# Performance work log

Hardware: AMD Instinct MI355X
Metric: run time of the kernel (lower is better)

The kernel has to match this reference:

```python
import math
import jax, jax.numpy as jnp
import numpy as np

B, N, CS, CZ, C, H, PQ, PV = 1, 768, 384, 128, 16, 12, 4, 8
INF, EPS = 100000.0, 1e-8
CONCAT = H * (CZ + C + PV * 4)  # 2112


def setup_inputs() -> dict:
    key = jax.random.key(0)
    ks = jax.random.split(key, 16)
    # random proper rotations via QR (numpy, deterministic)
    rng = np.random.default_rng(0)
    m = rng.standard_normal((B * N, 3, 3)).astype(np.float32)
    q, r = np.linalg.qr(m)
    q = q * np.sign(np.diagonal(r, axis1=-2, axis2=-1))[:, None, :]
    rot = jnp.asarray(q.reshape(B, N, 3, 3), dtype=jnp.float32)

    def lin(k, fin, fout):
        return jax.random.normal(k, (fin, fout), jnp.float32) / math.sqrt(fin)

    return {
        "s": jax.random.normal(ks[0], (B, N, CS), jnp.float32),
        "z": jax.random.normal(ks[1], (B, N, N, CZ), jnp.float32),
        "rot": rot,
        "trans": jax.random.normal(ks[2], (B, N, 3), jnp.float32),
        "mask": jnp.ones((B, N), jnp.float32),
        "Wq": lin(ks[3], CS, H * C), "bq": jnp.zeros((H * C,), jnp.float32),
        "Wkv": lin(ks[4], CS, 2 * H * C), "bkv": jnp.zeros((2 * H * C,), jnp.float32),
        "Wqp": lin(ks[5], CS, H * PQ * 3), "bqp": jnp.zeros((H * PQ * 3,), jnp.float32),
        "Wkvp": lin(ks[6], CS, H * (PQ + PV) * 3), "bkvp": jnp.zeros((H * (PQ + PV) * 3,), jnp.float32),
        "Wb": lin(ks[7], CZ, H), "bb": jnp.zeros((H,), jnp.float32),
        "head_w": jnp.full((H,), 0.541324854612918, jnp.float32),  # softplus^-1(1)
        "Wout": lin(ks[8], CONCAT, CS), "bout": jnp.zeros((CS,), jnp.float32),
    }


def reference(s, z, rot, trans, mask, Wq, bq, Wkv, bkv, Wqp, bqp, Wkvp, bkvp, Wb, bb, head_w, Wout, bout):
    q = (s @ Wq + bq).reshape(B, N, H, C)
    kv = (s @ Wkv + bkv).reshape(B, N, H, 2 * C)
    k, v = kv[..., :C], kv[..., C:]

    def to_points(lin_out, P):
        # torch split-into-3 + stack(dim=-1) layout: [.., 3, H*P] -> [.., H*P, 3]
        pts = lin_out.reshape(B, N, 3, H * P).swapaxes(-1, -2)
        pts = jnp.einsum('bnxy,bnpy->bnpx', rot, pts) + trans[:, :, None, :]
        return pts.reshape(B, N, H, P, 3)

    q_pts = to_points(s @ Wqp + bqp, PQ)
    kv_pts = to_points(s @ Wkvp + bkvp, PQ + PV)
    k_pts, v_pts = kv_pts[..., :PQ, :], kv_pts[..., PQ:, :]

    b = z @ Wb + bb  # [B,N,N,H]
    a = jnp.einsum('bihc,bjhc->bhij', q, k) * math.sqrt(1.0 / (3 * C))
    a = a + math.sqrt(1.0 / 3) * jnp.transpose(b, (0, 3, 1, 2))

    # point-distance attention: [B,N,N,H,PQ]
    d2 = jnp.sum((q_pts[:, :, None] - k_pts[:, None]) ** 2, axis=-1)
    hw = jax.nn.softplus(head_w) * math.sqrt(1.0 / (3 * (PQ * 9.0 / 2)))
    pt_att = -0.5 * jnp.sum(d2 * hw[:, None], axis=-1)  # [B,N,N,H]
    sq_mask = INF * (mask[:, :, None] * mask[:, None, :] - 1.0)
    a = a + jnp.transpose(pt_att, (0, 3, 1, 2)) + sq_mask[:, None]
    a = jax.nn.softmax(a, axis=-1)  # [B,H,N,N]

    o = jnp.einsum('bhij,bjhc->bihc', a, v).reshape(B, N, H * C)
    o_pt = jnp.einsum('bhij,bjhpx->bihpx', a, v_pts)  # [B,N,H,PV,3]
    # invert_apply: R^T (x - t)
    o_pt = jnp.einsum('bnyx,bnhpy->bnhpx', rot, o_pt - trans[:, :, None, None, :])
    o_pt_norm = jnp.sqrt(jnp.sum(o_pt ** 2, axis=-1) + EPS).reshape(B, N, H * PV)
    o_pt_flat = o_pt.reshape(B, N, H * PV, 3)
    o_pair = jnp.einsum('bhij,bijc->bihc', a, z).reshape(B, N, H * CZ)

    cat = jnp.concatenate(
        [o, o_pt_flat[..., 0], o_pt_flat[..., 1], o_pt_flat[..., 2], o_pt_norm, o_pair], axis=-1)
    return cat @ Wout + bout
```

## Files before the change

kernel.cpp:

```cpp
#include <hip/hip_runtime.h>
#include <math.h>

#define NN 768
#define CSn 384
#define CZn 128
#define Hn 12
#define CONCATn 2112
#define LGS 772

__global__ __launch_bounds__(256, 4) void projbias_kernel(
    const float* __restrict__ s,
    const float* __restrict__ Wq, const float* __restrict__ bq,
    const float* __restrict__ Wkv, const float* __restrict__ bkv,
    const float* __restrict__ Wqp, const float* __restrict__ bqp,
    const float* __restrict__ Wkvp, const float* __restrict__ bkvp,
    float* __restrict__ linG,
    const float* __restrict__ z, const float* __restrict__ Wb,
    const float* __restrict__ bb, float* __restrict__ bG)
{
    __shared__ float sl[16 * 388];
    __shared__ float wbs[1536];
    const int bid = blockIdx.x;
    const int t = threadIdx.x;

    if (bid < 864) {
        const int rt = bid % 48, ct = bid / 48;
        const int r0 = rt * 16;
        for (int x4 = t; x4 < 1536; x4 += 256) {
            const int r = x4 / 96, c4 = x4 % 96;
            *(float4*)&sl[r * 388 + c4 * 4] = *(const float4*)(s + (size_t)(r0 + r) * CSn + c4 * 4);
        }
        __syncthreads();
        const int c = t & 63, rq = t >> 6;
        const int col = ct * 64 + c;
        const float* Wp; int fout; float bias;
        if (col < 192)      { Wp = Wq + col;         fout = 192; bias = bq[col]; }
        else if (col < 576) { Wp = Wkv + (col-192);  fout = 384; bias = bkv[col-192]; }
        else if (col < 720) { Wp = Wqp + (col-576);  fout = 144; bias = bqp[col-576]; }
        else                { Wp = Wkvp + (col-720); fout = 432; bias = bkvp[col-720]; }
        float a0=bias, a1=bias, a2=bias, a3=bias;
        const float* s0 = sl + (rq*4+0)*388;
        const float* s1 = sl + (rq*4+1)*388;
        const float* s2 = sl + (rq*4+2)*388;
        const float* s3 = sl + (rq*4+3)*388;
        float wA[8], wB[8];
        #pragma unroll
        for (int u = 0; u < 8; ++u) wA[u] = Wp[(size_t)u * fout];
        #pragma unroll 1
        for (int kk = 0; kk < 384; kk += 16) {
            #pragma unroll
            for (int u = 0; u < 8; ++u) wB[u] = Wp[(size_t)(kk + 8 + u) * fout];
            #pragma unroll
            for (int u = 0; u < 8; ++u) {
                const float wv = wA[u];
                a0 += s0[kk+u]*wv; a1 += s1[kk+u]*wv;
                a2 += s2[kk+u]*wv; a3 += s3[kk+u]*wv;
            }
            if (kk + 16 < 384) {
                #pragma unroll
                for (int u = 0; u < 8; ++u) wA[u] = Wp[(size_t)(kk + 16 + u) * fout];
            }
            #pragma unroll
            for (int u = 0; u < 8; ++u) {
                const float wv = wB[u];
                a0 += s0[kk+8+u]*wv; a1 += s1[kk+8+u]*wv;
                a2 += s2[kk+8+u]*wv; a3 += s3[kk+8+u]*wv;
            }
        }
        float* lr = linG + (size_t)(r0 + rq*4) * 1152 + col;
        lr[0] = a0; lr[1152] = a1; lr[2*1152] = a2; lr[3*1152] = a3;
    } else {
        const int bb2 = bid - 864;
        const int jt = bb2 % 12, i = bb2 / 12;
        for (int x = t; x < 1536; x += 256) wbs[x] = Wb[(x & 127)*12 + (x >> 7)];
        __syncthreads();

        const int jl = t >> 2, g = t & 3;
        const int j = jt * 64 + jl;
        const float* zr = z + ((size_t)i * NN + j) * CZn + g * 4;
        float4 zv[8];
        #pragma unroll
        for (int u = 0; u < 8; ++u) zv[u] = *(const float4*)(zr + u * 16);

        float bh[12];
        #pragma unroll
        for (int h = 0; h < 12; ++h) bh[h] = 0.f;
        #pragma unroll
        for (int u = 0; u < 8; ++u) {
            const float* wb = wbs + u*16 + g*4;
            #pragma unroll
            for (int h = 0; h < 12; ++h) {
                const float4 wv = *(const float4*)(wb + h * 128);
                bh[h] += zv[u].x*wv.x + zv[u].y*wv.y + zv[u].z*wv.z + zv[u].w*wv.w;
            }
        }
        #pragma unroll
        for (int h = 0; h < 12; ++h) {
            bh[h] += __shfl_xor(bh[h], 1);
            bh[h] += __shfl_xor(bh[h], 2);
        }
        float bsel[3];
        #pragma unroll
        for (int hh = 0; hh < 3; ++hh) {
            const float v01 = (g & 1) ? bh[3+hh] : bh[0+hh];
            const float v23 = (g & 1) ? bh[9+hh] : bh[6+hh];
            bsel[hh] = (g & 2) ? v23 : v01;
        }
        float* bgr = bG + (size_t)i * (Hn*NN) + j;
        #pragma unroll
        for (int hh = 0; hh < 3; ++hh) {
            const int h = 3*g + hh;
            bgr[(size_t)h * NN] = 0.5773502691896258f * (bsel[hh] + bb[h]);
        }
    }
}

__global__ __launch_bounds__(256) void scatter_kernel(
    const float* __restrict__ linG, const float* __restrict__ rot, const float* __restrict__ trans,
    float* __restrict__ q, float* __restrict__ kT, float* __restrict__ v,
    float* __restrict__ qp, float* __restrict__ kpT, float* __restrict__ vp)
{
    const int i = blockIdx.x, t = threadIdx.x;
    const float* lr = linG + (size_t)i * 1152;
    if (t < 192) q[(size_t)i*192 + t] = lr[t];
    for (int tt = t; tt < 384; tt += 256) {
        const int h = tt >> 5, cc = tt & 31;
        const float val = lr[192 + tt];
        if (cc < 16) kT[(size_t)(h*16 + cc)*NN + i] = val;
        else         v[(size_t)i*192 + h*16 + (cc-16)] = val;
    }
    const float R0 = rot[i*9+0], R1 = rot[i*9+1], R2 = rot[i*9+2];
    const float R3 = rot[i*9+3], R4 = rot[i*9+4], R5 = rot[i*9+5];
    const float R6 = rot[i*9+6], R7 = rot[i*9+7], R8 = rot[i*9+8];
    const float T0 = trans[i*3+0], T1 = trans[i*3+1], T2 = trans[i*3+2];
    if (t < 48) {
        const float px = lr[576 + t], py = lr[576 + 48 + t], pz = lr[576 + 96 + t];
        float* d = qp + (size_t)i*144 + t*3;
        d[0] = R0*px + R1*py + R2*pz + T0;
        d[1] = R3*px + R4*py + R5*pz + T1;
        d[2] = R6*px + R7*py + R8*pz + T2;
    }
    if (t < 144) {
        const float px = lr[720 + t], py = lr[720 + 144 + t], pz = lr[720 + 288 + t];
        const float gx = R0*px + R1*py + R2*pz + T0;
        const float gy = R3*px + R4*py + R5*pz + T1;
        const float gz = R6*px + R7*py + R8*pz + T2;
        const int h = t / 12, pp = t % 12;
        if (pp < 4) {
            float* d = kpT + (size_t)(h*12 + pp*3)*NN + i;
            d[0] = gx; d[NN] = gy; d[2*NN] = gz;
        } else {
            float* d = vp + (size_t)i*288 + ((h*8) + (pp-4))*3;
            d[0] = gx; d[1] = gy; d[2] = gz;
        }
    }
}

#define LOADG(KV, KPV, BGv, MJv, uu) {                                        \
    const int jo_ = (uu) * 64;                                                \
    _Pragma("unroll") for (int c_ = 0; c_ < 16; ++c_)                         \
        KV[c_] = kb[(size_t)c_*NN + jo_];                                     \
    _Pragma("unroll") for (int e_ = 0; e_ < 12; ++e_)                         \
        KPV[e_] = kpb[(size_t)e_*NN + jo_];                                   \
    BGv = bgb[jo_]; MJv = mask[l + jo_]; }

#define COMPG(KV, KPV, BGv, MJv, uu) {                                        \
    float qk_ = 0.f;                                                          \
    _Pragma("unroll") for (int c_ = 0; c_ < 16; ++c_) qk_ += qreg[c_]*KV[c_]; \
    float d2_ = 0.f;                                                          \
    _Pragma("unroll") for (int e_ = 0; e_ < 12; ++e_) {                       \
        const float d_ = qpreg[e_] - KPV[e_]; d2_ += d_*d_; }                 \
    e[uu] = 0.14433756729740643f*qk_ + BGv + coef*d2_                         \
          + 100000.0f*(mi*MJv - 1.0f); }

__global__ __launch_bounds__(256, 3) void mega_kernel(
    const float* __restrict__ mask,
    const float* __restrict__ q, const float* __restrict__ qp,
    const float* __restrict__ kT, const float* __restrict__ kpT,
    const float* __restrict__ bG, const float* __restrict__ head_w,
    const float* __restrict__ z,
    const float* __restrict__ v, const float* __restrict__ vp,
    const float* __restrict__ rot, const float* __restrict__ trans,
    float* __restrict__ cat)
{
    const int i = blockIdx.x, t = threadIdx.x;
    const int w = t >> 6, l = t & 63;
    __shared__ float lg[Hn * LGS];
    __shared__ float qs[192], qps[144], coefS[12];
    __shared__ float pts[288];
    if (t < 192) qs[t] = q[(size_t)i*192 + t];
    if (t < 144) qps[t] = qp[(size_t)i*144 + t];
    if (t < 12) coefS[t] = -0.5f * 0.1360827634879543f * log1pf(expf(head_w[t]));
    __syncthreads();
    const float mi = mask[i];

    #pragma unroll 1
    for (int hh = 0; hh < 3; ++hh) {
        const int h = w*3 + hh;
        float qreg[16], qpreg[12];
        #pragma unroll
        for (int c = 0; c < 16; ++c) qreg[c] = qs[h*16 + c];
        #pragma unroll
        for (int ee = 0; ee < 12; ++ee) qpreg[ee] = qps[h*12 + ee];
        const float coef = coefS[h];
        const float* kb  = kT  + (size_t)(h*16)*NN + l;
        const float* kpb = kpT + (size_t)(h*12)*NN + l;
        const float* bgb = bG + (size_t)i*(Hn*NN) + (size_t)h*NN + l;
        float e[12];
        float kvA[16], kpvA[12], bgA, mjA;
        float kvB[16], kpvB[12], bgB, mjB;
        LOADG(kvA, kpvA, bgA, mjA, 0);
        #pragma unroll
        for (int u = 0; u < 12; u += 2) {
            LOADG(kvB, kpvB, bgB, mjB, u + 1);
            COMPG(kvA, kpvA, bgA, mjA, u);
            if (u + 2 < 12) LOADG(kvA, kpvA, bgA, mjA, u + 2);
            COMPG(kvB, kpvB, bgB, mjB, u + 1);
        }
        float m = -1e30f;
        #pragma unroll
        for (int u = 0; u < 12; ++u) m = fmaxf(m, e[u]);
        #pragma unroll
        for (int off = 32; off > 0; off >>= 1) m = fmaxf(m, __shfl_xor(m, off));
        float ssum = 0.f;
        #pragma unroll
        for (int u = 0; u < 12; ++u) { e[u] = expf(e[u] - m); ssum += e[u]; }
        #pragma unroll
        for (int off = 32; off > 0; off >>= 1) ssum += __shfl_xor(ssum, off);
        const float inv = 1.0f / ssum;
        #pragma unroll
        for (int u = 0; u < 12; ++u) lg[h*LGS + l + u*64] = e[u] * inv;
    }
    __syncthreads();

    {
        float accA = 0.f;
        const float* srcA; int strA; int hA;
        if (t < 192) { srcA = v + t;          strA = 192; hA = t >> 4; }
        else         { srcA = vp + (t - 192); strA = 288; hA = (t - 192) / 24; }
        const float* arA = lg + hA * LGS;
        {
            float vA[8], vB[8];
            #pragma unroll
            for (int u = 0; u < 8; ++u) vA[u] = srcA[(size_t)u * strA];
            #pragma unroll 1
            for (int jb = 0; jb < NN; jb += 16) {
                #pragma unroll
                for (int u = 0; u < 8; ++u) vB[u] = srcA[(size_t)(jb + 8 + u) * strA];
                #pragma unroll
                for (int u = 0; u < 8; ++u) accA += arA[jb + u] * vA[u];
                if (jb + 16 < NN) {
                    #pragma unroll
                    for (int u = 0; u < 8; ++u) vA[u] = srcA[(size_t)(jb + 16 + u) * strA];
                }
                #pragma unroll
                for (int u = 0; u < 8; ++u) accA += arA[jb + 8 + u] * vB[u];
            }
        }
        float accB = 0.f;
        if (t < 224) {
            const int cB = 64 + t;
            const float* srcB = vp + cB;
            const float* arB = lg + (cB / 24) * LGS;
            float vA[8], vB[8];
            #pragma unroll
            for (int u = 0; u < 8; ++u) vA[u] = srcB[(size_t)u * 288];
            #pragma unroll 1
            for (int jb = 0; jb < NN; jb += 16) {
                #pragma unroll
                for (int u = 0; u < 8; ++u) vB[u] = srcB[(size_t)(jb + 8 + u) * 288];
                #pragma unroll
                for (int u = 0; u < 8; ++u) accB += arB[jb + u] * vA[u];
                if (jb + 16 < NN) {
                    #pragma unroll
                    for (int u = 0; u < 8; ++u) vA[u] = srcB[(size_t)(jb + 16 + u) * 288];
                }
                #pragma unroll
                for (int u = 0; u < 8; ++u) accB += arB[jb + 8 + u] * vB[u];
            }
        }
        float* catr = cat + (size_t)i*CONCATn;
        if (t < 192) catr[t] = accA;
        else         pts[t - 192] = accA;
        if (t < 224) pts[64 + t] = accB;
    }
    __syncthreads();

    if (t < 96) {
        const float gx = pts[t*3+0] - trans[i*3+0];
        const float gy = pts[t*3+1] - trans[i*3+1];
        const float gz = pts[t*3+2] - trans[i*3+2];
        const float lx = rot[i*9+0]*gx + rot[i*9+3]*gy + rot[i*9+6]*gz;
        const float ly = rot[i*9+1]*gx + rot[i*9+4]*gy + rot[i*9+7]*gz;
        const float lz = rot[i*9+2]*gx + rot[i*9+5]*gy + rot[i*9+8]*gz;
        float* catr = cat + (size_t)i*CONCATn;
        catr[192 + t] = lx;
        catr[288 + t] = ly;
        catr[384 + t] = lz;
        catr[480 + t] = sqrtf(lx*lx + ly*ly + lz*lz + 1e-8f);
    }

    {
        const int c4 = l & 31, jp = l >> 5;
        const float* zb = z + (size_t)i*NN*CZn + c4*4;
        const float* a0 = lg + (size_t)(3*w + 0)*LGS;
        const float* a1 = lg + (size_t)(3*w + 1)*LGS;
        const float* a2 = lg + (size_t)(3*w + 2)*LGS;
        float x00=0.f,x01=0.f,x02=0.f,x03=0.f;
        float x10=0.f,x11=0.f,x12=0.f,x13=0.f;
        float x20=0.f,x21=0.f,x22=0.f,x23=0.f;
        float4 zA[8], zB[8];
        #pragma unroll
        for (int u = 0; u < 8; ++u)
            zA[u] = *(const float4*)(zb + (size_t)(2*u + jp)*CZn);
        #pragma unroll 1
        for (int jb = 0; jb < 384; jb += 16) {
            #pragma unroll
            for (int u = 0; u < 8; ++u)
                zB[u] = *(const float4*)(zb + (size_t)(2*(jb + 8 + u) + jp)*CZn);
            #pragma unroll
            for (int u = 0; u < 8; ++u) {
                const int j = 2*(jb + u) + jp;
                const float4 zv = zA[u];
                const float A0 = a0[j], A1 = a1[j], A2 = a2[j];
                x00 += A0*zv.x; x01 += A0*zv.y; x02 += A0*zv.z; x03 += A0*zv.w;
                x10 += A1*zv.x; x11 += A1*zv.y; x12 += A1*zv.z; x13 += A1*zv.w;
                x20 += A2*zv.x; x21 += A2*zv.y; x22 += A2*zv.z; x23 += A2*zv.w;
            }
            if (jb + 16 < 384) {
                #pragma unroll
                for (int u = 0; u < 8; ++u)
                    zA[u] = *(const float4*)(zb + (size_t)(2*(jb + 16 + u) + jp)*CZn);
            }
            #pragma unroll
            for (int u = 0; u < 8; ++u) {
                const int j = 2*(jb + 8 + u) + jp;
                const float4 zv = zB[u];
                const float A0 = a0[j], A1 = a1[j], A2 = a2[j];
                x00 += A0*zv.x; x01 += A0*zv.y; x02 += A0*zv.z; x03 += A0*zv.w;
                x10 += A1*zv.x; x11 += A1*zv.y; x12 += A1*zv.z; x13 += A1*zv.w;
                x20 += A2*zv.x; x21 += A2*zv.y; x22 += A2*zv.z; x23 += A2*zv.w;
            }
        }
        x00 += __shfl_xor(x00, 32); x01 += __shfl_xor(x01, 32);
        x02 += __shfl_xor(x02, 32); x03 += __shfl_xor(x03, 32);
        x10 += __shfl_xor(x10, 32); x11 += __shfl_xor(x11, 32);
        x12 += __shfl_xor(x12, 32); x13 += __shfl_xor(x13, 32);
        x20 += __shfl_xor(x20, 32); x21 += __shfl_xor(x21, 32);
        x22 += __shfl_xor(x22, 32); x23 += __shfl_xor(x23, 32);
        if (jp == 0) {
            float* cr = cat + (size_t)i*CONCATn + 576 + c4*4;
            float4 r0; r0.x=x00; r0.y=x01; r0.z=x02; r0.w=x03;
            float4 r1; r1.x=x10; r1.y=x11; r1.z=x12; r1.w=x13;
            float4 r2; r2.x=x20; r2.y=x21; r2.z=x22; r2.w=x23;
            *(float4*)(cr + (size_t)(3*w+0)*CZn) = r0;
            *(float4*)(cr + (size_t)(3*w+1)*CZn) = r1;
            *(float4*)(cr + (size_t)(3*w+2)*CZn) = r2;
        }
    }
}

__global__ __launch_bounds__(128) void outpart_kernel(
    const float* __restrict__ cat, const float* __restrict__ Wout,
    float* __restrict__ pbuf)
{
    const int rt = blockIdx.x;
    const int ot = blockIdx.y;
    const int qt = blockIdx.z;
    __shared__ float cl[4 * 528];
    const int r0 = rt * 4;
    const int kb = qt * 528;
    for (int idx = threadIdx.x; idx < 528; idx += 128) {
        const int r = idx / 132, c4 = idx % 132;
        *(float4*)&cl[r*528 + c4*4] =
            *(const float4*)(cat + (size_t)(r0 + r)*CONCATn + kb + c4*4);
    }
    __syncthreads();
    const int t = threadIdx.x;
    const int r  = t >> 5;
    const int o4 = t & 31;
    const int col = ot * 128 + o4 * 4;
    float4 acc; acc.x = 0.f; acc.y = 0.f; acc.z = 0.f; acc.w = 0.f;
    const float* wp = Wout + (size_t)kb * 384 + col;
    const float* cr = cl + r * 528;
    float4 wA[8], wB[8];
    #pragma unroll
    for (int u = 0; u < 8; ++u) wA[u] = *(const float4*)(wp + (size_t)u * 384);
    #pragma unroll 1
    for (int kk = 0; kk < 528; kk += 16) {
        #pragma unroll
        for (int u = 0; u < 8; ++u)
            wB[u] = *(const float4*)(wp + (size_t)(kk + 8 + u) * 384);
        #pragma unroll
        for (int u = 0; u < 8; ++u) {
            const float cv = cr[kk + u];
            acc.x += cv * wA[u].x; acc.y += cv * wA[u].y;
            acc.z += cv * wA[u].z; acc.w += cv * wA[u].w;
        }
        if (kk + 16 < 528) {
            #pragma unroll
            for (int u = 0; u < 8; ++u)
                wA[u] = *(const float4*)(wp + (size_t)(kk + 16 + u) * 384);
        }
        #pragma unroll
        for (int u = 0; u < 8; ++u) {
            const float cv = cr[kk + 8 + u];
            acc.x += cv * wB[u].x; acc.y += cv * wB[u].y;
            acc.z += cv * wB[u].z; acc.w += cv * wB[u].w;
        }
    }
    *(float4*)(pbuf + ((size_t)qt*NN + r0 + r)*384 + col) = acc;
}

__global__ __launch_bounds__(256) void outfin_kernel(
    const float* __restrict__ pbuf, const float* __restrict__ bout,
    float* __restrict__ out)
{
    const int idx4 = blockIdx.x * 256 + threadIdx.x;
    const int Q = NN * 384 / 4;
    const float4 p0 = ((const float4*)pbuf)[idx4];
    const float4 p1 = ((const float4*)pbuf)[idx4 + Q];
    const float4 p2 = ((const float4*)pbuf)[idx4 + 2*Q];
    const float4 p3 = ((const float4*)pbuf)[idx4 + 3*Q];
    const float4 bo = *(const float4*)(bout + (idx4 % 96) * 4);
    float4 r;
    r.x = p0.x + p1.x + p2.x + p3.x + bo.x;
    r.y = p0.y + p1.y + p2.y + p3.y + bo.y;
    r.z = p0.z + p1.z + p2.z + p3.z + bo.z;
    r.w = p0.w + p1.w + p2.w + p3.w + bo.w;
    ((float4*)out)[idx4] = r;
}

extern "C" void kernel_launch(void* const* d_in, const int* in_sizes, int n_in,
                              void* d_out, int out_size, void* d_ws, size_t ws_size,
                              hipStream_t stream)
{
    const float* s     = (const float*)d_in[0];
    const float* z     = (const float*)d_in[1];
    const float* rot   = (const float*)d_in[2];
    const float* trans = (const float*)d_in[3];
    const float* mask  = (const float*)d_in[4];
    const float* Wq    = (const float*)d_in[5];
    const float* bq    = (const float*)d_in[6];
    const float* Wkv   = (const float*)d_in[7];
    const float* bkv   = (const float*)d_in[8];
    const float* Wqp   = (const float*)d_in[9];
    const float* bqp   = (const float*)d_in[10];
    const float* Wkvp  = (const float*)d_in[11];
    const float* bkvp  = (const float*)d_in[12];
    const float* Wb    = (const float*)d_in[13];
    const float* bb    = (const float*)d_in[14];
    const float* head_w= (const float*)d_in[15];
    const float* Wout  = (const float*)d_in[16];
    const float* bout  = (const float*)d_in[17];
    float* out = (float*)d_out;

    float* ws    = (float*)d_ws;
    float* q     = ws;
    float* kT    = q     + 147456;
    float* qp    = kT    + 147456;
    float* kpT   = qp    + 110592;
    float* v     = kpT   + 110592;
    float* vp    = v     + 147456;
    float* cat   = vp    + 221184;
    float* linG  = cat   + 1622016;
    float* bG    = linG  + 884736;
    float* pbuf  = bG    + 7077888;

    hipLaunchKernelGGL(projbias_kernel, dim3(864 + 12*768), dim3(256), 0, stream,
        s, Wq, bq, Wkv, bkv, Wqp, bqp, Wkvp, bkvp, linG, z, Wb, bb, bG);
    hipLaunchKernelGGL(scatter_kernel, dim3(768), dim3(256), 0, stream,
        linG, rot, trans, q, kT, v, qp, kpT, vp);
    hipLaunchKernelGGL(mega_kernel, dim3(768), dim3(256), 0, stream,
        mask, q, qp, kT, kpT, bG, head_w, z, v, vp, rot, trans, cat);
    hipLaunchKernelGGL(outpart_kernel, dim3(192, 3, 4), dim3(128), 0, stream,
        cat, Wout, pbuf);
    hipLaunchKernelGGL(outfin_kernel, dim3(288), dim3(256), 0, stream,
        pbuf, bout, out);
}
```

Measured before the change: 352.4 us.

## Write q/k/v directly from projection kernel and simplify z-pair loop

The projection GEMM epilogue now writes q, transposed k, and v straight to their final layouts, so the scatter kernel handles only the point projections and linG shrinks to the point columns. This removes one global round trip for the scalar q/k/v data. Separately, the manual double-buffered z prefetch in the pair-output loop is replaced with a plain loop unrolled by 8, leaving load scheduling to the compiler. That lowers register pressure but may expose more memory latency. The kT writes from the epilogue are 4-wide contiguous per thread but strided across threads.

```diff
diff --git a/kernel.cpp b/kernel.cpp
--- a/kernel.cpp
+++ b/kernel.cpp
@@ -14,6 +14,7 @@
     const float* __restrict__ Wkv, const float* __restrict__ bkv,
     const float* __restrict__ Wqp, const float* __restrict__ bqp,
     const float* __restrict__ Wkvp, const float* __restrict__ bkvp,
+    float* __restrict__ q, float* __restrict__ kT, float* __restrict__ v,
     float* __restrict__ linG,
     const float* __restrict__ z, const float* __restrict__ Wb,
     const float* __restrict__ bb, float* __restrict__ bG)
@@ -67,8 +68,28 @@
                 a2 += s2[kk+8+u]*wv; a3 += s3[kk+8+u]*wv;
             }
         }
-        float* lr = linG + (size_t)(r0 + rq*4) * 1152 + col;
-        lr[0] = a0; lr[1152] = a1; lr[2*1152] = a2; lr[3*1152] = a3;
+        const int rb = r0 + rq*4;
+        if (col < 192) {
+            q[(size_t)(rb+0)*192 + col] = a0;
+            q[(size_t)(rb+1)*192 + col] = a1;
+            q[(size_t)(rb+2)*192 + col] = a2;
+            q[(size_t)(rb+3)*192 + col] = a3;
+        } else if (col < 576) {
+            const int tt = col - 192, h = tt >> 5, cc = tt & 31;
+            if (cc < 16) {
+                float* d = kT + (size_t)(h*16 + cc)*NN + rb;
+                d[0] = a0; d[1] = a1; d[2] = a2; d[3] = a3;
+            } else {
+                const int vc = h*16 + (cc - 16);
+                v[(size_t)(rb+0)*192 + vc] = a0;
+                v[(size_t)(rb+1)*192 + vc] = a1;
+                v[(size_t)(rb+2)*192 + vc] = a2;
+                v[(size_t)(rb+3)*192 + vc] = a3;
+            }
+        } else {
+            float* lr = linG + (size_t)rb * 576 + (col - 576);
+            lr[0] = a0; lr[576] = a1; lr[2*576] = a2; lr[3*576] = a3;
+        }
     } else {
         const int bb2 = bid - 864;
         const int jt = bb2 % 12, i = bb2 / 12;
@@ -115,33 +136,25 @@
     }
 }
 
-__global__ __launch_bounds__(256) void scatter_kernel(
+__global__ __launch_bounds__(256) void pts_scatter_kernel(
     const float* __restrict__ linG, const float* __restrict__ rot, const float* __restrict__ trans,
-    float* __restrict__ q, float* __restrict__ kT, float* __restrict__ v,
     float* __restrict__ qp, float* __restrict__ kpT, float* __restrict__ vp)
 {
     const int i = blockIdx.x, t = threadIdx.x;
-    const float* lr = linG + (size_t)i * 1152;
-    if (t < 192) q[(size_t)i*192 + t] = lr[t];
-    for (int tt = t; tt < 384; tt += 256) {
-        const int h = tt >> 5, cc = tt & 31;
-        const float val = lr[192 + tt];
-        if (cc < 16) kT[(size_t)(h*16 + cc)*NN + i] = val;
-        else         v[(size_t)i*192 + h*16 + (cc-16)] = val;
-    }
+    const float* lr = linG + (size_t)i * 576;
     const float R0 = rot[i*9+0], R1 = rot[i*9+1], R2 = rot[i*9+2];
     const float R3 = rot[i*9+3], R4 = rot[i*9+4], R5 = rot[i*9+5];
     const float R6 = rot[i*9+6], R7 = rot[i*9+7], R8 = rot[i*9+8];
     const float T0 = trans[i*3+0], T1 = trans[i*3+1], T2 = trans[i*3+2];
     if (t < 48) {
-        const float px = lr[576 + t], py = lr[576 + 48 + t], pz = lr[576 + 96 + t];
+        const float px = lr[t], py = lr[48 + t], pz = lr[96 + t];
         float* d = qp + (size_t)i*144 + t*3;
         d[0] = R0*px + R1*py + R2*pz + T0;
         d[1] = R3*px + R4*py + R5*pz + T1;
         d[2] = R6*px + R7*py + R8*pz + T2;
     }
     if (t < 144) {
-        const float px = lr[720 + t], py = lr[720 + 144 + t], pz = lr[720 + 288 + t];
+        const float px = lr[144 + t], py = lr[288 + t], pz = lr[432 + t];
         const float gx = R0*px + R1*py + R2*pz + T0;
         const float gy = R3*px + R4*py + R5*pz + T1;
         const float gz = R6*px + R7*py + R8*pz + T2;
@@ -309,38 +322,14 @@
         float x00=0.f,x01=0.f,x02=0.f,x03=0.f;
         float x10=0.f,x11=0.f,x12=0.f,x13=0.f;
         float x20=0.f,x21=0.f,x22=0.f,x23=0.f;
-        float4 zA[8], zB[8];
-        #pragma unroll
-        for (int u = 0; u < 8; ++u)
-            zA[u] = *(const float4*)(zb + (size_t)(2*u + jp)*CZn);
-        #pragma unroll 1
-        for (int jb = 0; jb < 384; jb += 16) {
-            #pragma unroll
-            for (int u = 0; u < 8; ++u)
-                zB[u] = *(const float4*)(zb + (size_t)(2*(jb + 8 + u) + jp)*CZn);
-            #pragma unroll
-            for (int u = 0; u < 8; ++u) {
-                const int j = 2*(jb + u) + jp;
-                const float4 zv = zA[u];
-                const float A0 = a0[j], A1 = a1[j], A2 = a2[j];
-                x00 += A0*zv.x; x01 += A0*zv.y; x02 += A0*zv.z; x03 += A0*zv.w;
-                x10 += A1*zv.x; x11 += A1*zv.y; x12 += A1*zv.z; x13 += A1*zv.w;
-                x20 += A2*zv.x; x21 += A2*zv.y; x22 += A2*zv.z; x23 += A2*zv.w;
-            }
-            if (jb + 16 < 384) {
-                #pragma unroll
-                for (int u = 0; u < 8; ++u)
-                    zA[u] = *(const float4*)(zb + (size_t)(2*(jb + 16 + u) + jp)*CZn);
-            }
-            #pragma unroll
-            for (int u = 0; u < 8; ++u) {
-                const int j = 2*(jb + 8 + u) + jp;
-                const float4 zv = zB[u];
-                const float A0 = a0[j], A1 = a1[j], A2 = a2[j];
-                x00 += A0*zv.x; x01 += A0*zv.y; x02 += A0*zv.z; x03 += A0*zv.w;
-                x10 += A1*zv.x; x11 += A1*zv.y; x12 += A1*zv.z; x13 += A1*zv.w;
-                x20 += A2*zv.x; x21 += A2*zv.y; x22 += A2*zv.z; x23 += A2*zv.w;
-            }
+        #pragma unroll 8
+        for (int j2 = 0; j2 < 384; ++j2) {
+            const int j = 2*j2 + jp;
+            const float4 zv = *(const float4*)(zb + (size_t)j*CZn);
+            const float A0 = a0[j], A1 = a1[j], A2 = a2[j];
+            x00 += A0*zv.x; x01 += A0*zv.y; x02 += A0*zv.z; x03 += A0*zv.w;
+            x10 += A1*zv.x; x11 += A1*zv.y; x12 += A1*zv.z; x13 += A1*zv.w;
+            x20 += A2*zv.x; x21 += A2*zv.y; x22 += A2*zv.z; x23 += A2*zv.w;
         }
         x00 += __shfl_xor(x00, 32); x01 += __shfl_xor(x01, 32);
         x02 += __shfl_xor(x02, 32); x03 += __shfl_xor(x03, 32);
@@ -464,13 +453,13 @@
     float* vp    = v     + 147456;
     float* cat   = vp    + 221184;
     float* linG  = cat   + 1622016;
-    float* bG    = linG  + 884736;
+    float* bG    = linG  + 442368;
     float* pbuf  = bG    + 7077888;
 
     hipLaunchKernelGGL(projbias_kernel, dim3(864 + 12*768), dim3(256), 0, stream,
-        s, Wq, bq, Wkv, bkv, Wqp, bqp, Wkvp, bkvp, linG, z, Wb, bb, bG);
-    hipLaunchKernelGGL(scatter_kernel, dim3(768), dim3(256), 0, stream,
-        linG, rot, trans, q, kT, v, qp, kpT, vp);
+        s, Wq, bq, Wkv, bkv, Wqp, bqp, Wkvp, bkvp, q, kT, v, linG, z, Wb, bb, bG);
+    hipLaunchKernelGGL(pts_scatter_kernel, dim3(768), dim3(256), 0, stream,
+        linG, rot, trans, qp, kpT, vp);
     hipLaunchKernelGGL(mega_kernel, dim3(768), dim3(256), 0, stream,
         mask, q, qp, kT, kpT, bG, head_w, z, v, vp, rot, trans, cat);
     hipLaunchKernelGGL(outpart_kernel, dim3(192, 3, 4), dim3(128), 0, stream,
```

After: 359.3 us. No clear change (+2.0%).
